# Optimization experiments

Hardware: AMD Instinct MI355X
Metric: run time of the kernel (lower is better)

Reference implementation:

```python
import jax, jax.numpy as jnp
import numpy as np

WEIGHT_SCALE = 0.02  # matches torch.randn(...)*0.02 init

def setup_inputs() -> dict:
    key = jax.random.key(0)
    k1, k2, k3, k4 = jax.random.split(key, 4)
    B, D = 16384, 1024
    x_re = jax.random.normal(k1, (B, D), dtype=jnp.float32)
    x_im = jax.random.normal(k2, (B, D), dtype=jnp.float32)
    w_re = jax.random.normal(k3, (D, D), dtype=jnp.float32) * WEIGHT_SCALE
    w_im = jax.random.normal(k4, (D, D), dtype=jnp.float32) * WEIGHT_SCALE
    return {"x_re": x_re, "x_im": x_im, "w_re": w_re, "w_im": w_im}

def reference(x_re, x_im, w_re, w_im):
    x = jax.lax.complex(x_re, x_im)            # [B, D] complex64
    W = jax.lax.complex(w_re, w_im)            # [D, D] complex64
    # Skew-Hermitian part: A = W - W^H
    A = W - jnp.conj(W.T)
    D = W.shape[0]
    I = jnp.eye(D, dtype=W.dtype)
    # Cayley transform: U = (I - A)^{-1} (I + A)  (unitary)
    U = jnp.linalg.solve(I - A, I + A)
    # Original: x @ U.transpose(-1, -2) (plain transpose, no conj)
    return x @ U.T
```

## Files before the change

### kernel.cpp

```cpp
#include <hip/hip_runtime.h>
#include <hip/hip_bf16.h>

#define DD 1024
#define NB 16384
#define SZ (DD * DD)
#define CHB 512

typedef unsigned short u16;
typedef __attribute__((ext_vector_type(4))) float f32x4;
typedef __attribute__((ext_vector_type(8))) short short8;
typedef __attribute__((ext_vector_type(4))) short short4v;

__device__ __forceinline__ u16 f32_bf16(float f) {
  unsigned u = __builtin_bit_cast(unsigned, f);
  u += 0x7FFFu + ((u >> 16) & 1u);
  return (u16)(u >> 16);
}
__device__ __forceinline__ float bf16_f32(u16 h) {
  unsigned u = ((unsigned)h) << 16;
  return __builtin_bit_cast(float, u);
}
__device__ __forceinline__ void gload16(const void* g, void* l) {
  __builtin_amdgcn_global_load_lds(
      (const __attribute__((address_space(1))) unsigned int*)g,
      (__attribute__((address_space(3))) unsigned int*)l, 16, 0, 0);
}

struct CArgs {
  const u16 *Ar[3], *Ai[3];
  const u16 *Br[3], *Bi[3];
  int nseg;
  float alpha, g1, g2, ddiag;
  const u16 *e1r, *e1i, *e2r, *e2i;
  u16 *hi_n_re, *hi_n_im, *lo_n_re, *lo_n_im;
  u16 *t1_re, *t1_im;
  u16 *t2_re, *t2_im;
  u16 *lt_re, *lt_im;
  int t_ldt;
  unsigned t1_xi;
  const float *cxr, *cxi; u16 *cxb;
  int cm0a, cm1a, cm0b, cm1b;
};

__global__ __launch_bounds__(256) void zchain(CArgs g) {
  constexpr int SA = 64 * 32, SB = 32 * 32;
  constexpr int SLOT = 2 * SA + 2 * SB;
  __shared__ __align__(16) u16 smem[4 * SLOT];
  const int tid = threadIdx.x;

  if ((int)blockIdx.x >= CHB) {
    int nra = g.cm1a - g.cm0a;
    int tot = nra + (g.cm1b - g.cm0b);
    for (int r = (int)blockIdx.x - CHB; r < tot; r += 256) {
      int m = (r < nra) ? (g.cm0a + r) : (g.cm0b + r - nra);
      f32x4 v = ((const f32x4*)g.cxr)[m * 256 + tid];
      short4v s;
      #pragma unroll
      for (int e = 0; e < 4; ++e) s[e] = (short)f32_bf16(v[e]);
      ((short4v*)g.cxb)[m * 512 + tid] = s;
      f32x4 w = ((const f32x4*)g.cxi)[m * 256 + tid];
      #pragma unroll
      for (int e = 0; e < 4; ++e) s[e] = (short)f32_bf16(w[e]);
      ((short4v*)g.cxb)[m * 512 + 256 + tid] = s;
    }
    return;
  }

  const int lane = tid & 63, wave = tid >> 6;
  const int wr = wave >> 1, wc = wave & 1;
  const int l15 = lane & 15, lg = lane >> 4;

  { }
  const int lin = blockIdx.x;
  const int xcd = lin & 7, tt = lin >> 3;
  const int by = (xcd >> 2) * 8 + (tt >> 3);
  const int bx = (xcd & 3) * 8 + (tt & 7);
  const int m0 = by * 64, n0 = bx * 32;

  const int arow = tid >> 2, agc = tid & 3;
  const int offA = (m0 + arow) * DD + ((agc ^ ((arow >> 1) & 3)) * 8);
  const int ldsA = tid * 8;
  const int bplane = tid >> 7, bcc = tid & 127;
  const int brow = bcc >> 2, bgc = bcc & 3;
  const int offB = (n0 + brow) * DD + ((bgc ^ ((brow >> 1) & 3)) * 8);
  const int ldsB = 2 * SA + bplane * SB + bcc * 8;

  const int slotR = lg ^ ((l15 >> 1) & 3);
  int frA[2];
  #pragma unroll
  for (int mf = 0; mf < 2; ++mf)
    frA[mf] = (wr * 32 + mf * 16 + l15) * 32 + slotR * 8;
  const int frB = (wc * 16 + l15) * 32 + slotR * 8;

  const int nt = g.nseg * 32;

  auto ISSUE = [&](int b) {
    if (b >= nt) return;
    int s = b >> 5, kk = (b & 31) << 5;
    u16* base = smem + (b & 3) * SLOT;
    gload16(g.Ar[s] + offA + kk, base + ldsA);
    gload16(g.Ai[s] + offA + kk, base + SA + ldsA);
    const u16* bptr = bplane ? g.Bi[s] : g.Br[s];
    gload16(bptr + offB + kk, base + ldsB);
  };

  f32x4 accre[2] = {};
  f32x4 accim[2] = {};

  ISSUE(0); ISSUE(1); ISSUE(2);
  asm volatile("s_waitcnt vmcnt(6)" ::: "memory");
  __builtin_amdgcn_s_barrier();

  for (int b = 0; b < nt; ++b) {
    ISSUE(b + 3);
    const u16* base = smem + (b & 3) * SLOT;
    short8 ar[2], ai[2];
    #pragma unroll
    for (int mf = 0; mf < 2; ++mf) {
      ar[mf] = *(const short8*)(base + frA[mf]);
      ai[mf] = *(const short8*)(base + SA + frA[mf]);
    }
    short8 br = *(const short8*)(base + 2 * SA + frB);
    short8 bi = *(const short8*)(base + 2 * SA + SB + frB);
    short8 bin;
    #pragma unroll
    for (int e = 0; e < 8; ++e) bin[e] = (short)(bi[e] ^ (short)0x8000);
    __builtin_amdgcn_s_setprio(1);
    #pragma unroll
    for (int mf = 0; mf < 2; ++mf) {
      accre[mf] = __builtin_amdgcn_mfma_f32_16x16x32_bf16(ar[mf], br,  accre[mf], 0, 0, 0);
      accre[mf] = __builtin_amdgcn_mfma_f32_16x16x32_bf16(ai[mf], bin, accre[mf], 0, 0, 0);
      accim[mf] = __builtin_amdgcn_mfma_f32_16x16x32_bf16(ar[mf], bi,  accim[mf], 0, 0, 0);
      accim[mf] = __builtin_amdgcn_mfma_f32_16x16x32_bf16(ai[mf], br,  accim[mf], 0, 0, 0);
    }
    __builtin_amdgcn_s_setprio(0);
    int rem = nt - 1 - b;
    if (rem >= 3)      asm volatile("s_waitcnt vmcnt(6)" ::: "memory");
    else if (rem == 2) asm volatile("s_waitcnt vmcnt(3)" ::: "memory");
    else if (rem == 1) asm volatile("s_waitcnt vmcnt(0)" ::: "memory");
    if (rem) __builtin_amdgcn_s_barrier();
  }

  u16 hre[2][4], hie[2][4], lre[2][4], lie[2][4];
  #pragma unroll
  for (int mf = 0; mf < 2; ++mf)
  #pragma unroll
  for (int r = 0; r < 4; ++r) {
    int gr = m0 + wr * 32 + mf * 16 + lg * 4 + r;
    int gc = n0 + wc * 16 + l15;
    size_t idx = (size_t)gr * DD + gc;
    float v = g.alpha * accre[mf][r];
    float w = g.alpha * accim[mf][r];
    if (g.e1r) { v += g.g1 * bf16_f32(g.e1r[idx]); w += g.g1 * bf16_f32(g.e1i[idx]); }
    if (g.e2r) { v += g.g2 * bf16_f32(g.e2r[idx]); w += g.g2 * bf16_f32(g.e2i[idx]); }
    if (gr == gc) v += g.ddiag;
    u16 h1 = f32_bf16(v); hre[mf][r] = h1;
    u16 h2 = f32_bf16(w); hie[mf][r] = h2;
    lre[mf][r] = f32_bf16(v - bf16_f32(h1));
    lie[mf][r] = f32_bf16(w - bf16_f32(h2));
    if (g.hi_n_re) { g.hi_n_re[idx] = h1; g.hi_n_im[idx] = h2; }
    if (g.lo_n_re) { g.lo_n_re[idx] = lre[mf][r]; g.lo_n_im[idx] = lie[mf][r]; }
  }

  auto bounce = [&](u16 (&vals)[2][4], u16* outp, unsigned xorm) {
    if (!outp) return;
    __syncthreads();
    #pragma unroll
    for (int mf = 0; mf < 2; ++mf)
    #pragma unroll
    for (int r = 0; r < 4; ++r) {
      int row = wr * 32 + mf * 16 + lg * 4 + r;
      int col = wc * 16 + l15;
      smem[row * 34 + col] = vals[mf][r];
    }
    __syncthreads();
    if (tid < 128) {
      int col = tid & 31, mb = (tid >> 5) * 16;
      short8 s0, s1;
      #pragma unroll
      for (int j = 0; j < 8; ++j) s0[j] = (short)(smem[(mb + j) * 34 + col] ^ xorm);
      #pragma unroll
      for (int j = 0; j < 8; ++j) s1[j] = (short)(smem[(mb + 8 + j) * 34 + col] ^ xorm);
      u16* p = outp + (size_t)(n0 + col) * g.t_ldt + m0 + mb;
      *(short8*)p = s0; *(short8*)(p + 8) = s1;
    }
  };

  bounce(hre, g.t1_re, 0);
  bounce(hie, g.t1_im, g.t1_xi);
  bounce(hre, g.t2_re, 0);
  bounce(hie, g.t2_im, 0);
  bounce(lre, g.lt_re, 0);
  bounce(lie, g.lt_im, 0);
}

#define RG_SA (256 * 32)
#define RG_SB (256 * 32)
#define RG_SLOT (RG_SA + RG_SB)
#define RG_LDS_BYTES (4 * RG_SLOT * 2)
#define RG_NT 64

__global__ __launch_bounds__(512, 2) void rgemm(
    const u16* __restrict__ A, const u16* __restrict__ B,
    float* __restrict__ out, int ostride, int ooff)
{
  extern __shared__ u16 smem[];
  const int tid = threadIdx.x, lane = tid & 63, wave = tid >> 6;
  const int wr = wave >> 2, wc = wave & 3;
  const int l15 = lane & 15, lg = lane >> 4;

  int bx, by;
  { int lin = blockIdx.y * gridDim.x + blockIdx.x;
    int orig = (lin & 7) * 32 + (lin >> 3);
    bx = orig & 3; by = orig >> 2; }
  const int m0 = by * 256, n0 = bx * 256;

  int offA[2], ldsA[2], offB[2], ldsB[2];
  #pragma unroll
  for (int i = 0; i < 2; ++i) {
    int c = i * 512 + tid; int row = c >> 2; int q = c & 3;
    offA[i] = (m0 + row) * 2048 + ((q ^ ((row >> 1) & 3)) * 8);
    ldsA[i] = c * 8;
    offB[i] = (n0 + row) * 2048 + ((q ^ ((row >> 1) & 3)) * 8);
    ldsB[i] = RG_SA + c * 8;
  }

  const int slotR = lg ^ ((l15 >> 1) & 3);
  int ra[8], rb[4];
  #pragma unroll
  for (int mf = 0; mf < 8; ++mf) ra[mf] = (wr * 128 + mf * 16 + l15) * 32 + slotR * 8;
  #pragma unroll
  for (int nf = 0; nf < 4; ++nf) rb[nf] = RG_SA + (wc * 64 + nf * 16 + l15) * 32 + slotR * 8;

  auto ISSUE = [&](int b) {
    if (b >= RG_NT) return;
    int kk = b << 5;
    u16* base = smem + (b & 3) * RG_SLOT;
    #pragma unroll
    for (int i = 0; i < 2; ++i) {
      gload16(A + offA[i] + kk, base + ldsA[i]);
      gload16(B + offB[i] + kk, base + ldsB[i]);
    }
  };

  f32x4 acc[8][4] = {};

  ISSUE(0); ISSUE(1); ISSUE(2);
  asm volatile("s_waitcnt vmcnt(8)" ::: "memory");
  __builtin_amdgcn_s_barrier();

  for (int b = 0; b < RG_NT; ++b) {
    ISSUE(b + 3);
    const u16* base = smem + (b & 3) * RG_SLOT;
    short8 bb[4];
    #pragma unroll
    for (int nf = 0; nf < 4; ++nf) bb[nf] = *(const short8*)(base + rb[nf]);
    #pragma unroll
    for (int mf = 0; mf < 8; ++mf) {
      short8 av = *(const short8*)(base + ra[mf]);
      __builtin_amdgcn_s_setprio(1);
      #pragma unroll
      for (int nf = 0; nf < 4; ++nf)
        acc[mf][nf] = __builtin_amdgcn_mfma_f32_16x16x32_bf16(av, bb[nf], acc[mf][nf], 0, 0, 0);
      __builtin_amdgcn_s_setprio(0);
    }
    int rem = RG_NT - 1 - b;
    if (rem >= 3)      asm volatile("s_waitcnt vmcnt(8)" ::: "memory");
    else if (rem == 2) asm volatile("s_waitcnt vmcnt(4)" ::: "memory");
    else if (rem == 1) asm volatile("s_waitcnt vmcnt(0)" ::: "memory");
    if (rem) __builtin_amdgcn_s_barrier();
  }

  #pragma unroll
  for (int mf = 0; mf < 8; ++mf)
  #pragma unroll
  for (int nf = 0; nf < 4; ++nf)
  #pragma unroll
  for (int r = 0; r < 4; ++r) {
    int gr = m0 + wr * 128 + mf * 16 + lg * 4 + r;
    int gc = n0 + wc * 64 + nf * 16 + l15;
    out[((size_t)gr * DD + gc) * ostride + ooff] = acc[mf][nf][r];
  }
}

__global__ __launch_bounds__(256) void prep_w(
    const float* __restrict__ wre, const float* __restrict__ wim,
    u16* Shr, u16* Shi_, u16* Slr, u16* Sli, u16* Snr)
{
  __shared__ float tr[32][33], ti[32][33];
  const int tx = threadIdx.x, ty = threadIdx.y;
  const int bx = blockIdx.x, by = blockIdx.y;
  #pragma unroll
  for (int k = 0; k < 4; ++k) {
    int r = bx * 32 + ty + 8 * k, c = by * 32 + tx;
    tr[ty + 8 * k][tx] = wre[r * DD + c];
    ti[ty + 8 * k][tx] = wim[r * DD + c];
  }
  __syncthreads();
  #pragma unroll
  for (int k = 0; k < 4; ++k) {
    int i = by * 32 + ty + 8 * k, j = bx * 32 + tx;
    float wr_ij = wre[i * DD + j], wi_ij = wim[i * DD + j];
    float wr_ji = tr[tx][ty + 8 * k], wi_ji = ti[tx][ty + 8 * k];
    float Sre = wr_ji - wr_ij;
    float Sim = wi_ij + wi_ji;
    int idx = i * DD + j;
    u16 h1 = f32_bf16(Sre); Shr[idx] = h1; Slr[idx] = f32_bf16(Sre - bf16_f32(h1));
    u16 h2 = f32_bf16(Sim); Shi_[idx] = h2; Sli[idx] = f32_bf16(Sim - bf16_f32(h2));
    Snr[idx] = (u16)(h1 ^ 0x8000u);
  }
}

__global__ __launch_bounds__(256) void prep_x2(
    const float* __restrict__ xr, const float* __restrict__ xi,
    u16* __restrict__ xb, int m0a, int m1a, int m0b, int m1b)
{
  int nra = m1a - m0a;
  int tot = nra + (m1b - m0b);
  const int tid = threadIdx.x;
  for (int r = blockIdx.x; r < tot; r += gridDim.x) {
    int m = (r < nra) ? (m0a + r) : (m0b + r - nra);
    f32x4 v = ((const f32x4*)xr)[m * 256 + tid];
    short4v s;
    #pragma unroll
    for (int e = 0; e < 4; ++e) s[e] = (short)f32_bf16(v[e]);
    ((short4v*)xb)[m * 512 + tid] = s;
    f32x4 w = ((const f32x4*)xi)[m * 256 + tid];
    #pragma unroll
    for (int e = 0; e < 4; ++e) s[e] = (short)f32_bf16(w[e]);
    ((short4v*)xb)[m * 512 + 256 + tid] = s;
  }
}

extern "C" void kernel_launch(void* const* d_in, const int* in_sizes, int n_in,
                              void* d_out, int out_size, void* d_ws, size_t ws_size,
                              hipStream_t stream)
{
  const float* xr  = (const float*)d_in[0];
  const float* xi  = (const float*)d_in[1];
  const float* wre = (const float*)d_in[2];
  const float* wim = (const float*)d_in[3];
  const bool realOut = (out_size == NB * DD);

  u16* P0 = (u16*)d_ws;
  auto PL = [&](int k) { return P0 + (size_t)k * SZ; };
  u16 *Shr = PL(0), *Shi_ = PL(1), *Slr = PL(2), *Sli = PL(3), *Snr = PL(4);
  u16 *Cn_r = PL(5), *Cn_i = PL(6), *Ct_r = PL(7), *Ct_i = PL(8);
  u16 *Rn_r = PL(9), *Rn_i = PL(10);
  u16 *XA_hn_r = PL(11), *XA_hn_i = PL(12), *XA_ht_r = PL(13), *XA_ht_i = PL(14);
  u16 *XB_hn_r = PL(19), *XB_hn_i = PL(20), *XB_ht_r = PL(21), *XB_ht_i = PL(22);
  u16 *XB_ln_r = PL(23), *XB_ln_i = PL(24), *XB_lt_r = PL(25), *XB_lt_i = PL(26);
  u16 *T_ht_r = PL(29), *T_ht_i = PL(30), *T_lt_r = PL(31), *T_lt_i = PL(32);
  u16 *pack1 = PL(33);
  u16 *pack2 = PL(35);
  u16 *xb    = PL(0);

  dim3 blk(256);
  prep_w<<<dim3(32, 32), dim3(32, 8), 0, stream>>>(
      wre, wim, Shr, Shi_, Slr, Sli, Snr);

  auto chain = [&](CArgs& a, int p0, int p1, int p0b, int p1b) {
    a.cxr = xr; a.cxi = xi; a.cxb = xb;
    a.cm0a = p0 * 512; a.cm1a = p1 * 512;
    a.cm0b = p0b * 512; a.cm1b = p1b * 512;
    zchain<<<dim3(CHB + 256), blk, 0, stream>>>(a);
  };
  auto base = [&]() { CArgs a{}; a.nseg = 1; a.t_ldt = DD; return a; };

  { CArgs a = base();
    a.Ar[0] = Shr; a.Ai[0] = Shi_; a.Br[0] = Snr; a.Bi[0] = Shi_;
    a.alpha = 1.f;
    a.hi_n_re = Cn_r; a.hi_n_im = Cn_i; a.t1_re = Ct_r; a.t1_im = Ct_i;
    chain(a, 15, 19, 0, 0); }
  { CArgs a = base();
    a.Ar[0] = Cn_r; a.Ai[0] = Cn_i; a.Br[0] = Ct_r; a.Bi[0] = Ct_i;
    a.alpha = 0.0212604f; a.g1 = 0.2381155f; a.e1r = Cn_r; a.e1i = Cn_i;
    a.ddiag = 0.7910964f;
    a.hi_n_re = Rn_r; a.hi_n_im = Rn_i;
    chain(a, 27, 29, 0, 0); }
  { CArgs a = base();
    a.Ar[0] = Rn_r; a.Ai[0] = Rn_i; a.Br[0] = Snr; a.Bi[0] = Shi_;
    a.alpha = 1.f; a.g1 = 1.f; a.e1r = Rn_r; a.e1i = Rn_i;
    a.hi_n_re = XA_hn_r; a.hi_n_im = XA_hn_i; a.t1_re = XA_ht_r; a.t1_im = XA_ht_i;
    chain(a, 0, 0, 0, 0); }
  { CArgs a = base();
    a.Ar[0] = Shr; a.Ai[0] = Shi_; a.Br[0] = XA_ht_r; a.Bi[0] = XA_ht_i;
    a.alpha = -1.f; a.g1 = 1.f; a.e1r = XA_hn_r; a.e1i = XA_hn_i;
    a.t1_re = T_ht_r; a.t1_im = T_ht_i;
    chain(a, 4, 8, 0, 0); }
  { CArgs a = base();
    a.Ar[0] = XA_hn_r; a.Ai[0] = XA_hn_i; a.Br[0] = T_ht_r; a.Bi[0] = T_ht_i;
    a.alpha = -1.f; a.g1 = 2.f; a.e1r = XA_hn_r; a.e1i = XA_hn_i;
    a.hi_n_re = XB_hn_r; a.hi_n_im = XB_hn_i; a.t1_re = XB_ht_r; a.t1_im = XB_ht_i;
    a.lo_n_re = XB_ln_r; a.lo_n_im = XB_ln_i; a.lt_re = XB_lt_r; a.lt_im = XB_lt_i;
    chain(a, 8, 11, 0, 0); }
  { CArgs a = base();
    a.nseg = 3;
    a.Ar[0] = Shr; a.Ai[0] = Shi_; a.Br[0] = XB_ht_r; a.Bi[0] = XB_ht_i;
    a.Ar[1] = Shr; a.Ai[1] = Shi_; a.Br[1] = XB_lt_r; a.Bi[1] = XB_lt_i;
    a.Ar[2] = Slr; a.Ai[2] = Sli;  a.Br[2] = XB_ht_r; a.Bi[2] = XB_ht_i;
    a.alpha = -1.f;
    a.g1 = 1.f; a.e1r = XB_hn_r; a.e1i = XB_hn_i;
    a.g2 = 1.f; a.e2r = XB_ln_r; a.e2i = XB_ln_i;
    a.t1_re = T_ht_r; a.t1_im = T_ht_i; a.lt_re = T_lt_r; a.lt_im = T_lt_i;
    chain(a, 11, 15, 0, 0); }
  { CArgs a = base();
    a.nseg = 2;
    a.Ar[0] = XB_hn_r; a.Ai[0] = XB_hn_i; a.Br[0] = T_ht_r; a.Bi[0] = T_ht_i;
    a.Ar[1] = XB_hn_r; a.Ai[1] = XB_hn_i; a.Br[1] = T_lt_r; a.Bi[1] = T_lt_i;
    a.alpha = -2.f;
    a.g1 = 4.f; a.e1r = XB_hn_r; a.e1i = XB_hn_i;
    a.g2 = 2.f; a.e2r = XB_ln_r; a.e2i = XB_ln_i;
    a.ddiag = -1.f;
    a.t_ldt = 2048;
    a.t1_re = pack1; a.t1_im = pack1 + 1024; a.t1_xi = 0x8000u;
    if (!realOut) { a.t2_im = pack2; a.t2_re = pack2 + 1024; }
    chain(a, 0, 4, 0, 0); }

  prep_x2<<<dim3(1024), blk, 0, stream>>>(
      xr, xi, xb, 19 * 512, 27 * 512, 29 * 512, 32 * 512);

  (void)hipFuncSetAttribute((const void*)rgemm,
      hipFuncAttributeMaxDynamicSharedMemorySize, RG_LDS_BYTES);
  dim3 gB(DD / 256, NB / 256);
  if (realOut) {
    rgemm<<<gB, dim3(512), RG_LDS_BYTES, stream>>>(xb, pack1, (float*)d_out, 1, 0);
  } else {
    rgemm<<<gB, dim3(512), RG_LDS_BYTES, stream>>>(xb, pack1, (float*)d_out, 2, 0);
    rgemm<<<gB, dim3(512), RG_LDS_BYTES, stream>>>(xb, pack2, (float*)d_out, 2, 1);
  }
}
```

Before: 327.5 us.

## Split GEMM k-step into two phases interleaving LDS reads, global prefetch and MFMA

Restructures the main GEMM loop into two half-phases. Each phase reads a batch of A fragments from LDS, issues half of the next tile's global-to-LDS loads (A or B), synchronises with a barrier, then runs a 4x4 block of MFMAs at raised priority. The goal is to spread memory issue across the iteration and overlap LDS reads and global loads with MFMA work, ping-pong style. In exchange it adds two extra barriers per iteration, and the new barriers could create stalls if the waves drift out of step.

```diff
diff --git a/kernel.cpp b/kernel.cpp
--- a/kernel.cpp
+++ b/kernel.cpp
@@ -232,38 +232,59 @@
   #pragma unroll
   for (int nf = 0; nf < 4; ++nf) rb[nf] = RG_SA + (wc * 64 + nf * 16 + l15) * 32 + slotR * 8;
 
-  auto ISSUE = [&](int b) {
+  auto ISSUE_A = [&](int b) {
     if (b >= RG_NT) return;
     int kk = b << 5;
     u16* base = smem + (b & 3) * RG_SLOT;
     #pragma unroll
-    for (int i = 0; i < 2; ++i) {
-      gload16(A + offA[i] + kk, base + ldsA[i]);
-      gload16(B + offB[i] + kk, base + ldsB[i]);
-    }
+    for (int i = 0; i < 2; ++i) gload16(A + offA[i] + kk, base + ldsA[i]);
   };
+  auto ISSUE_B = [&](int b) {
+    if (b >= RG_NT) return;
+    int kk = b << 5;
+    u16* base = smem + (b & 3) * RG_SLOT;
+    #pragma unroll
+    for (int i = 0; i < 2; ++i) gload16(B + offB[i] + kk, base + ldsB[i]);
+  };
 
   f32x4 acc[8][4] = {};
 
-  ISSUE(0); ISSUE(1); ISSUE(2);
+  ISSUE_A(0); ISSUE_B(0);
+  ISSUE_A(1); ISSUE_B(1);
+  ISSUE_A(2); ISSUE_B(2);
   asm volatile("s_waitcnt vmcnt(8)" ::: "memory");
   __builtin_amdgcn_s_barrier();
 
   for (int b = 0; b < RG_NT; ++b) {
-    ISSUE(b + 3);
     const u16* base = smem + (b & 3) * RG_SLOT;
-    short8 bb[4];
+    short8 bb[4], av[4];
     #pragma unroll
     for (int nf = 0; nf < 4; ++nf) bb[nf] = *(const short8*)(base + rb[nf]);
     #pragma unroll
-    for (int mf = 0; mf < 8; ++mf) {
-      short8 av = *(const short8*)(base + ra[mf]);
-      __builtin_amdgcn_s_setprio(1);
+    for (int mf = 0; mf < 4; ++mf) av[mf] = *(const short8*)(base + ra[mf]);
+    ISSUE_A(b + 3);
+    __builtin_amdgcn_s_barrier();
+    asm volatile("s_waitcnt lgkmcnt(0)" ::: "memory");
+    __builtin_amdgcn_s_setprio(1);
+    #pragma unroll
+    for (int mf = 0; mf < 4; ++mf)
       #pragma unroll
       for (int nf = 0; nf < 4; ++nf)
-        acc[mf][nf] = __builtin_amdgcn_mfma_f32_16x16x32_bf16(av, bb[nf], acc[mf][nf], 0, 0, 0);
-      __builtin_amdgcn_s_setprio(0);
-    }
+        acc[mf][nf] = __builtin_amdgcn_mfma_f32_16x16x32_bf16(av[mf], bb[nf], acc[mf][nf], 0, 0, 0);
+    __builtin_amdgcn_s_setprio(0);
+    __builtin_amdgcn_s_barrier();
+    #pragma unroll
+    for (int mf = 0; mf < 4; ++mf) av[mf] = *(const short8*)(base + ra[4 + mf]);
+    ISSUE_B(b + 3);
+    __builtin_amdgcn_s_barrier();
+    asm volatile("s_waitcnt lgkmcnt(0)" ::: "memory");
+    __builtin_amdgcn_s_setprio(1);
+    #pragma unroll
+    for (int mf = 0; mf < 4; ++mf)
+      #pragma unroll
+      for (int nf = 0; nf < 4; ++nf)
+        acc[4 + mf][nf] = __builtin_amdgcn_mfma_f32_16x16x32_bf16(av[mf], bb[nf], acc[4 + mf][nf], 0, 0, 0);
+    __builtin_amdgcn_s_setprio(0);
     int rem = RG_NT - 1 - b;
     if (rem >= 3)      asm volatile("s_waitcnt vmcnt(8)" ::: "memory");
     else if (rem == 2) asm volatile("s_waitcnt vmcnt(4)" ::: "memory");
```

Measured after the change: 327.5 us. About the same (+0.0%).

## Restructure rgemm into a double-buffered K=64 pipeline with quadrant-staged loads

Applied to the files above, without the earlier changes.

Rewrites the main bf16 GEMM mainloop. The old version was a 4-slot ring of K=32 tiles. The new one uses two LDS buffers of K=64 tiles with an XOR-swizzled 64-column layout. Each tile is split into four MFMA quadrants, and the global->LDS loads for the next tiles are interleaved between those quadrants, separated by barriers and raised wave priority. The aim is to overlap memory traffic with MFMA work more finely and to halve the number of loop iterations and barriers per K step. The cost is more barriers per tile and a more fragile hand-written wait-count schedule.

```diff
diff --git a/kernel.cpp b/kernel.cpp
--- a/kernel.cpp
+++ b/kernel.cpp
@@ -70,7 +70,6 @@
   const int wr = wave >> 1, wc = wave & 1;
   const int l15 = lane & 15, lg = lane >> 4;
 
-  { }
   const int lin = blockIdx.x;
   const int xcd = lin & 7, tt = lin >> 3;
   const int by = (xcd >> 2) * 8 + (tt >> 3);
@@ -194,11 +193,9 @@
   bounce(lie, g.lt_im, 0);
 }
 
-#define RG_SA (256 * 32)
-#define RG_SB (256 * 32)
-#define RG_SLOT (RG_SA + RG_SB)
-#define RG_LDS_BYTES (4 * RG_SLOT * 2)
-#define RG_NT 64
+#define RG_SLOT2 (2 * 256 * 64)
+#define RG_LDS_BYTES (2 * RG_SLOT2 * 2)
+#define RG_TILES 32
 
 __global__ __launch_bounds__(512, 2) void rgemm(
     const u16* __restrict__ A, const u16* __restrict__ B,
@@ -215,61 +212,136 @@
     bx = orig & 3; by = orig >> 2; }
   const int m0 = by * 256, n0 = bx * 256;
 
-  int offA[2], ldsA[2], offB[2], ldsB[2];
+  const u16* __restrict__ Abase = A + (size_t)m0 * 2048;
+  const u16* __restrict__ Bbase = B + (size_t)n0 * 2048;
+
+  int gofsA[2], gofsB[2], lofs[2];
   #pragma unroll
   for (int i = 0; i < 2; ++i) {
-    int c = i * 512 + tid; int row = c >> 2; int q = c & 3;
-    offA[i] = (m0 + row) * 2048 + ((q ^ ((row >> 1) & 3)) * 8);
-    ldsA[i] = c * 8;
-    offB[i] = (n0 + row) * 2048 + ((q ^ ((row >> 1) & 3)) * 8);
-    ldsB[i] = RG_SA + c * 8;
-  }
-
-  const int slotR = lg ^ ((l15 >> 1) & 3);
-  int ra[8], rb[4];
-  #pragma unroll
-  for (int mf = 0; mf < 8; ++mf) ra[mf] = (wr * 128 + mf * 16 + l15) * 32 + slotR * 8;
-  #pragma unroll
-  for (int nf = 0; nf < 4; ++nf) rb[nf] = RG_SA + (wc * 64 + nf * 16 + l15) * 32 + slotR * 8;
-
-  auto ISSUE = [&](int b) {
-    if (b >= RG_NT) return;
-    int kk = b << 5;
-    u16* base = smem + (b & 3) * RG_SLOT;
-    #pragma unroll
-    for (int i = 0; i < 2; ++i) {
-      gload16(A + offA[i] + kk, base + ldsA[i]);
-      gload16(B + offB[i] + kk, base + ldsB[i]);
-    }
+    int c = i * 512 + tid;
+    int sub = c >> 3;
+    int sl = (c & 7) ^ (sub & 7);
+    int rowA = (sub & 63) + 128 * (sub >> 6);
+    int rowB = (sub & 31) + 64 * (sub >> 5);
+    gofsA[i] = rowA * 2048 + sl * 8;
+    gofsB[i] = rowB * 2048 + sl * 8;
+    lofs[i] = c * 8;
+  }
+
+  int raf[8], rbf[8];
+  #pragma unroll
+  for (int mf = 0; mf < 4; ++mf)
+    #pragma unroll
+    for (int k = 0; k < 2; ++k)
+      raf[mf * 2 + k] = (wr * 64 + mf * 16 + l15) * 64 +
+                        (((k * 4 + lg) ^ (l15 & 7)) * 8);
+  #pragma unroll
+  for (int nf = 0; nf < 2; ++nf)
+    #pragma unroll
+    for (int k = 0; k < 2; ++k)
+      rbf[nf * 2 + k] = (wc * 32 + nf * 16 + l15) * 64 +
+                        (((k * 4 + lg) ^ (l15 & 7)) * 8);
+
+  f32x4 acc[8][4] = {};
+  short8 aA[8], bb[8];
+
+#define MFMA_Q(mb, nb)                                                        \
+  _Pragma("unroll")                                                           \
+  for (int mf = 0; mf < 4; ++mf)                                              \
+    _Pragma("unroll")                                                         \
+    for (int nf = 0; nf < 2; ++nf)                                            \
+      _Pragma("unroll")                                                       \
+      for (int k = 0; k < 2; ++k)                                             \
+        acc[(mb) + mf][(nb) + nf] = __builtin_amdgcn_mfma_f32_16x16x32_bf16(  \
+            aA[mf * 2 + k], bb[((nb) + nf) * 2 + k], acc[(mb) + mf][(nb) + nf], 0, 0, 0);
+
+  {
+    gload16(Abase + gofsA[0], smem + lofs[0]);
+    gload16(Abase + gofsA[1], smem + lofs[1]);
+    gload16(Bbase + gofsB[0], smem + 16384 + lofs[0]);
+    gload16(Bbase + gofsB[1], smem + 16384 + lofs[1]);
+    gload16(Bbase + gofsB[0] + 32 * 2048, smem + 16384 + 8192 + lofs[0]);
+    gload16(Bbase + gofsB[1] + 32 * 2048, smem + 16384 + 8192 + lofs[1]);
+    gload16(Abase + gofsA[0] + 64 * 2048, smem + 8192 + lofs[0]);
+    gload16(Abase + gofsA[1] + 64 * 2048, smem + 8192 + lofs[1]);
+    gload16(Abase + gofsA[0] + 64, smem + RG_SLOT2 + lofs[0]);
+    gload16(Abase + gofsA[1] + 64, smem + RG_SLOT2 + lofs[1]);
+    gload16(Bbase + gofsB[0] + 64, smem + RG_SLOT2 + 16384 + lofs[0]);
+    gload16(Bbase + gofsB[1] + 64, smem + RG_SLOT2 + 16384 + lofs[1]);
+  }
+  asm volatile("s_waitcnt vmcnt(4)" ::: "memory");
+  __builtin_amdgcn_s_barrier();
+
+  auto TILE = [&](int t, int gate, bool st01, bool st23) {
+    const int b = t & 1;
+    const u16* bA = smem + b * RG_SLOT2;
+    const u16* bB = bA + 16384;
+    u16* sOpp  = smem + (b ^ 1) * RG_SLOT2;
+    u16* sSame = smem + b * RG_SLOT2;
+    #pragma unroll
+    for (int i = 0; i < 8; ++i) aA[i] = *(const short8*)(bA + raf[i]);
+    #pragma unroll
+    for (int i = 0; i < 4; ++i) bb[i] = *(const short8*)(bB + rbf[i]);
+    if (st01) {
+      int kk = (t + 1) * 64;
+      gload16(Bbase + gofsB[0] + 32 * 2048 + kk, sOpp + 16384 + 8192 + lofs[0]);
+      gload16(Bbase + gofsB[1] + 32 * 2048 + kk, sOpp + 16384 + 8192 + lofs[1]);
+    }
+    asm volatile("s_waitcnt lgkmcnt(8)" ::: "memory");
+    __builtin_amdgcn_s_barrier();
+    asm volatile("s_waitcnt lgkmcnt(0)" ::: "memory");
+    __builtin_amdgcn_sched_barrier(0);
+    __builtin_amdgcn_s_setprio(1);
+    MFMA_Q(0, 0);
+    __builtin_amdgcn_s_setprio(0);
+    __builtin_amdgcn_s_barrier();
+    #pragma unroll
+    for (int i = 0; i < 4; ++i) bb[4 + i] = *(const short8*)(bB + 8192 + rbf[i]);
+    if (st01) {
+      int kk = (t + 1) * 64;
+      gload16(Abase + gofsA[0] + 64 * 2048 + kk, sOpp + 8192 + lofs[0]);
+      gload16(Abase + gofsA[1] + 64 * 2048 + kk, sOpp + 8192 + lofs[1]);
+    }
+    __builtin_amdgcn_s_barrier();
+    asm volatile("s_waitcnt lgkmcnt(0)" ::: "memory");
+    __builtin_amdgcn_sched_barrier(0);
+    __builtin_amdgcn_s_setprio(1);
+    MFMA_Q(0, 2);
+    __builtin_amdgcn_s_setprio(0);
+    __builtin_amdgcn_s_barrier();
+    #pragma unroll
+    for (int i = 0; i < 8; ++i) aA[i] = *(const short8*)(bA + 8192 + raf[i]);
+    if (st23) {
+      int kk = (t + 2) * 64;
+      gload16(Abase + gofsA[0] + kk, sSame + lofs[0]);
+      gload16(Abase + gofsA[1] + kk, sSame + lofs[1]);
+    }
+    __builtin_amdgcn_s_barrier();
+    asm volatile("s_waitcnt lgkmcnt(0)" ::: "memory");
+    __builtin_amdgcn_sched_barrier(0);
+    __builtin_amdgcn_s_setprio(1);
+    MFMA_Q(4, 0);
+    __builtin_amdgcn_s_setprio(0);
+    __builtin_amdgcn_s_barrier();
+    if (st23) {
+      int kk = (t + 2) * 64;
+      gload16(Bbase + gofsB[0] + kk, sSame + 16384 + lofs[0]);
+      gload16(Bbase + gofsB[1] + kk, sSame + 16384 + lofs[1]);
+    }
+    __builtin_amdgcn_s_barrier();
+    __builtin_amdgcn_sched_barrier(0);
+    __builtin_amdgcn_s_setprio(1);
+    MFMA_Q(4, 2);
+    __builtin_amdgcn_s_setprio(0);
+    if (gate == 4)      asm volatile("s_waitcnt vmcnt(4)" ::: "memory");
+    else if (gate == 0) asm volatile("s_waitcnt vmcnt(0)" ::: "memory");
+    if (gate >= 0) __builtin_amdgcn_s_barrier();
   };
 
-  f32x4 acc[8][4] = {};
-
-  ISSUE(0); ISSUE(1); ISSUE(2);
-  asm volatile("s_waitcnt vmcnt(8)" ::: "memory");
-  __builtin_amdgcn_s_barrier();
-
-  for (int b = 0; b < RG_NT; ++b) {
-    ISSUE(b + 3);
-    const u16* base = smem + (b & 3) * RG_SLOT;
-    short8 bb[4];
-    #pragma unroll
-    for (int nf = 0; nf < 4; ++nf) bb[nf] = *(const short8*)(base + rb[nf]);
-    #pragma unroll
-    for (int mf = 0; mf < 8; ++mf) {
-      short8 av = *(const short8*)(base + ra[mf]);
-      __builtin_amdgcn_s_setprio(1);
-      #pragma unroll
-      for (int nf = 0; nf < 4; ++nf)
-        acc[mf][nf] = __builtin_amdgcn_mfma_f32_16x16x32_bf16(av, bb[nf], acc[mf][nf], 0, 0, 0);
-      __builtin_amdgcn_s_setprio(0);
-    }
-    int rem = RG_NT - 1 - b;
-    if (rem >= 3)      asm volatile("s_waitcnt vmcnt(8)" ::: "memory");
-    else if (rem == 2) asm volatile("s_waitcnt vmcnt(4)" ::: "memory");
-    else if (rem == 1) asm volatile("s_waitcnt vmcnt(0)" ::: "memory");
-    if (rem) __builtin_amdgcn_s_barrier();
-  }
+  for (int t = 0; t < RG_TILES - 2; ++t) TILE(t, 4, true, true);
+  TILE(RG_TILES - 2, 0, true, false);
+  TILE(RG_TILES - 1, -1, false, false);
+#undef MFMA_Q
 
   #pragma unroll
   for (int mf = 0; mf < 8; ++mf)
```

Measured after the change: 323.1 us. Within noise of the previous version (-1.4%).
